# Kernel optimization log

Measured on AMD Instinct MI355X. Metric: run time of the kernel, lower is better.

Reference implementation:

```python
import jax, jax.numpy as jnp
import numpy as np

LN_EPS = 1e-5


def setup_inputs() -> dict:
    key = jax.random.key(0)
    ks = jax.random.split(key, 8)
    B, DIM = 65536, 768
    feat = jax.random.normal(ks[0], (B, 2, DIM), dtype=jnp.float32)
    s = 1.0 / np.sqrt(DIM)
    W_int = jax.random.uniform(ks[1], (9, DIM), minval=-s, maxval=s, dtype=jnp.float32)
    W_stim = jax.random.uniform(ks[2], (9, DIM), minval=-s, maxval=s, dtype=jnp.float32)
    trans = jax.random.uniform(ks[3], (9, 9, 9), dtype=jnp.float32)  # torch.rand init
    ln_w = jnp.ones((9,), dtype=jnp.float32)
    ln_b = jnp.zeros((9,), dtype=jnp.float32)
    so = 1.0 / np.sqrt(18)
    W_out = jax.random.uniform(ks[4], (9, 18), minval=-so, maxval=so, dtype=jnp.float32)
    b_out = jax.random.uniform(ks[5], (9,), minval=-so, maxval=so, dtype=jnp.float32)
    return {"feat": feat, "W_int": W_int, "W_stim": W_stim, "trans": trans,
            "ln_w": ln_w, "ln_b": ln_b, "W_out": W_out, "b_out": b_out}


def reference(feat, W_int, W_stim, trans, ln_w, ln_b, W_out, b_out):
    # last_feat = intensity(feat[:,0,:]); this_feat = stimulation(feat[:,1,:])
    last = feat[:, 0, :] @ W_int.T   # [B, 9]
    this = feat[:, 1, :] @ W_stim.T  # [B, 9]
    # per-sample: temp[a,k] = sum_j last[j]*trans[a,j,k]; out[k] = sum_a this[a]*temp[a,k]
    # batched trilinear contraction replaces the Python loop:
    bil = jnp.einsum('ba,bj,ajk->bk', this, last, trans)  # [B, 9]
    # LayerNorm(9)
    mu = jnp.mean(bil, axis=-1, keepdims=True)
    var = jnp.mean(jnp.square(bil - mu), axis=-1, keepdims=True)
    ln = (bil - mu) * jax.lax.rsqrt(var + LN_EPS) * ln_w + ln_b
    cat = jnp.concatenate([this, ln], axis=1)  # [B, 18]
    return cat @ W_out.T + b_out  # [B, 9]
```

## Files before the change

kernel.cpp:

```cpp
#include <hip/hip_runtime.h>

#define LN_EPS 1e-5f

constexpr int DIM   = 768;
constexpr int R     = 4;
constexpr int WAVES = 8;
constexpr int BLOCK = WAVES * 64;

__launch_bounds__(BLOCK, 1)
__global__ void fused_concat_linear(const float* __restrict__ feat,
                                    const float* __restrict__ W_int,
                                    const float* __restrict__ W_stim,
                                    const float* __restrict__ trans,
                                    const float* __restrict__ ln_w,
                                    const float* __restrict__ ln_b,
                                    const float* __restrict__ W_out,
                                    const float* __restrict__ b_out,
                                    float* __restrict__ out,
                                    int B)
{
    __shared__ float sW[2 * 9 * DIM];
    __shared__ float sTr[729];
    __shared__ float sWo[162];
    __shared__ float sBo[9];
    __shared__ float sLw[9];
    __shared__ float sLb[9];

    const int tid = threadIdx.x;
    {
        const float4* srcI = (const float4*)W_int;
        const float4* srcS = (const float4*)W_stim;
        float4* dst = (float4*)sW;
        constexpr int NW4 = (9 * DIM) / 4;
        for (int i = tid; i < NW4; i += BLOCK) {
            dst[i]       = srcI[i];
            dst[i + NW4] = srcS[i];
        }
        for (int i = tid; i < 729; i += BLOCK) sTr[i] = trans[i];
        if (tid < 162) sWo[tid] = W_out[tid];
        if (tid < 9) { sBo[tid] = b_out[tid]; sLw[tid] = ln_w[tid]; sLb[tid] = ln_b[tid]; }
    }
    __syncthreads();

    const int lane = tid & 63;
    const int wave = tid >> 6;
    const int r0 = (blockIdx.x * WAVES + wave) * R;

    int rows[R];
#pragma unroll
    for (int r = 0; r < R; ++r) rows[r] = min(r0 + r, B - 1);

    float acc_i[R][9];
    float acc_s[R][9];
#pragma unroll
    for (int r = 0; r < R; ++r)
#pragma unroll
        for (int a = 0; a < 9; ++a) { acc_i[r][a] = 0.f; acc_s[r][a] = 0.f; }

#pragma unroll
    for (int t = 0; t < 3; ++t) {
        const int base = t * 256 + lane * 4;
        float4 f0[R], f1[R];
#pragma unroll
        for (int r = 0; r < R; ++r) {
            const float* p = feat + (size_t)rows[r] * (2 * DIM);
            f0[r] = *(const float4*)(p + base);
            f1[r] = *(const float4*)(p + DIM + base);
        }
#pragma unroll
        for (int a = 0; a < 9; ++a) {
            const float4 wi = *(const float4*)(sW + a * DIM + base);
            const float4 ws = *(const float4*)(sW + 9 * DIM + a * DIM + base);
#pragma unroll
            for (int r = 0; r < R; ++r) {
                float ai = acc_i[r][a];
                ai = fmaf(f0[r].x, wi.x, ai);
                ai = fmaf(f0[r].y, wi.y, ai);
                ai = fmaf(f0[r].z, wi.z, ai);
                ai = fmaf(f0[r].w, wi.w, ai);
                acc_i[r][a] = ai;
                float as = acc_s[r][a];
                as = fmaf(f1[r].x, ws.x, as);
                as = fmaf(f1[r].y, ws.y, as);
                as = fmaf(f1[r].z, ws.z, as);
                as = fmaf(f1[r].w, ws.w, as);
                acc_s[r][a] = as;
            }
        }
    }

#pragma unroll
    for (int off = 32; off > 0; off >>= 1) {
#pragma unroll
        for (int r = 0; r < R; ++r)
#pragma unroll
            for (int a = 0; a < 9; ++a) {
                acc_i[r][a] += __shfl_xor(acc_i[r][a], off, 64);
                acc_s[r][a] += __shfl_xor(acc_s[r][a], off, 64);
            }
    }

    int rr = lane / 9;
    const int k = lane - rr * 9;
    const bool active = (rr < R);
    if (!active) rr = 0;

    float thisv[9], lastv[9];
#pragma unroll
    for (int a = 0; a < 9; ++a) {
        float tv = acc_s[0][a], lv = acc_i[0][a];
        tv = (rr == 1) ? acc_s[1][a] : tv;  lv = (rr == 1) ? acc_i[1][a] : lv;
        tv = (rr == 2) ? acc_s[2][a] : tv;  lv = (rr == 2) ? acc_i[2][a] : lv;
        tv = (rr == 3) ? acc_s[3][a] : tv;  lv = (rr == 3) ? acc_i[3][a] : lv;
        thisv[a] = tv; lastv[a] = lv;
    }

    float bil = 0.f;
#pragma unroll
    for (int a = 0; a < 9; ++a) {
        const float ta = thisv[a];
#pragma unroll
        for (int j = 0; j < 9; ++j) {
            bil = fmaf(ta * lastv[j], sTr[a * 81 + j * 9 + k], bil);
        }
    }

    const int rbase = rr * 9;
    float bilv[9];
#pragma unroll
    for (int j = 0; j < 9; ++j) bilv[j] = __shfl(bil, rbase + j, 64);

    float mu = 0.f;
#pragma unroll
    for (int j = 0; j < 9; ++j) mu += bilv[j];
    mu *= (1.f / 9.f);
    float var = 0.f;
#pragma unroll
    for (int j = 0; j < 9; ++j) { const float d = bilv[j] - mu; var = fmaf(d, d, var); }
    var *= (1.f / 9.f);
    const float rs = rsqrtf(var + LN_EPS);

    float o = sBo[k];
#pragma unroll
    for (int a = 0; a < 9; ++a) o = fmaf(thisv[a], sWo[k * 18 + a], o);
#pragma unroll
    for (int j = 0; j < 9; ++j) {
        const float lnj = fmaf((bilv[j] - mu) * rs, sLw[j], sLb[j]);
        o = fmaf(lnj, sWo[k * 18 + 9 + j], o);
    }

    const int row = r0 + rr;
    if (active && row < B) out[(size_t)row * 9 + k] = o;
}

extern "C" void kernel_launch(void* const* d_in, const int* in_sizes, int n_in,
                              void* d_out, int out_size, void* d_ws, size_t ws_size,
                              hipStream_t stream) {
    const float* feat   = (const float*)d_in[0];
    const float* W_int  = (const float*)d_in[1];
    const float* W_stim = (const float*)d_in[2];
    const float* trans  = (const float*)d_in[3];
    const float* ln_w   = (const float*)d_in[4];
    const float* ln_b   = (const float*)d_in[5];
    const float* W_out  = (const float*)d_in[6];
    const float* b_out  = (const float*)d_in[7];
    float* out = (float*)d_out;

    const int B = in_sizes[0] / (2 * DIM);
    const int rows_per_block = WAVES * R;
    const int grid = (B + rows_per_block - 1) / rows_per_block;

    fused_concat_linear<<<grid, BLOCK, 0, stream>>>(
        feat, W_int, W_stim, trans, ln_w, ln_b, W_out, b_out, out, B);
}
```

Before: 597.5 us.

## Map one row per lane and split DIM across waves with scalar weight loads

Work is remapped so each lane owns one batch row and each of four waves handles a quarter of the feature dimension. The wave-uniform weight addresses let the compiler use scalar loads straight from global memory, so the weights are no longer staged in LDS. This removes the 55 KB LDS preload per block and the long cross-lane shuffle reduction. Partial sums are now combined through a small LDS buffer, and wave 0 runs the bilinear, LayerNorm and output stages per row. The tradeoff is that per-lane feature loads now stride by a full row, which may hurt coalescing and L1 efficiency, and the epilogue runs on only one wave.

Measured after the change: 561.0 us. 6.1% less time.

```diff
diff --git a/kernel.cpp b/kernel.cpp
--- a/kernel.cpp
+++ b/kernel.cpp
@@ -2,12 +2,14 @@
 
 #define LN_EPS 1e-5f
 
-constexpr int DIM   = 768;
-constexpr int R     = 4;
-constexpr int WAVES = 8;
-constexpr int BLOCK = WAVES * 64;
+constexpr int DIM    = 768;
+constexpr int NSPLIT = 4;
+constexpr int BLOCK  = NSPLIT * 64;
+constexpr int SEG    = DIM / NSPLIT;
+constexpr int C      = 32;
+constexpr int NCHUNK = SEG / C;
 
-__launch_bounds__(BLOCK, 1)
+__launch_bounds__(BLOCK, 4)
 __global__ void fused_concat_linear(const float* __restrict__ feat,
                                     const float* __restrict__ W_int,
                                     const float* __restrict__ W_stim,
@@ -19,138 +21,114 @@
                                     float* __restrict__ out,
                                     int B)
 {
-    __shared__ float sW[2 * 9 * DIM];
-    __shared__ float sTr[729];
-    __shared__ float sWo[162];
-    __shared__ float sBo[9];
-    __shared__ float sLw[9];
-    __shared__ float sLb[9];
+    __shared__ float sP[NSPLIT][18][64];
 
-    const int tid = threadIdx.x;
-    {
-        const float4* srcI = (const float4*)W_int;
-        const float4* srcS = (const float4*)W_stim;
-        float4* dst = (float4*)sW;
-        constexpr int NW4 = (9 * DIM) / 4;
-        for (int i = tid; i < NW4; i += BLOCK) {
-            dst[i]       = srcI[i];
-            dst[i + NW4] = srcS[i];
-        }
-        for (int i = tid; i < 729; i += BLOCK) sTr[i] = trans[i];
-        if (tid < 162) sWo[tid] = W_out[tid];
-        if (tid < 9) { sBo[tid] = b_out[tid]; sLw[tid] = ln_w[tid]; sLb[tid] = ln_b[tid]; }
-    }
-    __syncthreads();
+    const int lane = threadIdx.x & 63;
+    const int wave = __builtin_amdgcn_readfirstlane(threadIdx.x >> 6);
 
-    const int lane = tid & 63;
-    const int wave = tid >> 6;
-    const int r0 = (blockIdx.x * WAVES + wave) * R;
+    const int row = blockIdx.x * 64 + lane;
+    const int rr  = min(row, B - 1);
+    const float* frow = feat + (size_t)rr * (2 * DIM);
 
-    int rows[R];
+    float accL[9], accT[9];
 #pragma unroll
-    for (int r = 0; r < R; ++r) rows[r] = min(r0 + r, B - 1);
-
-    float acc_i[R][9];
-    float acc_s[R][9];
-#pragma unroll
-    for (int r = 0; r < R; ++r)
-#pragma unroll
-        for (int a = 0; a < 9; ++a) { acc_i[r][a] = 0.f; acc_s[r][a] = 0.f; }
+    for (int a = 0; a < 9; ++a) { accL[a] = 0.f; accT[a] = 0.f; }
 
 #pragma unroll
-    for (int t = 0; t < 3; ++t) {
-        const int base = t * 256 + lane * 4;
-        float4 f0[R], f1[R];
+    for (int ch = 0; ch < NCHUNK; ++ch) {
+        const int c0 = wave * SEG + ch * C;
+
+        float4 f0[8], f1[8];
 #pragma unroll
-        for (int r = 0; r < R; ++r) {
-            const float* p = feat + (size_t)rows[r] * (2 * DIM);
-            f0[r] = *(const float4*)(p + base);
-            f1[r] = *(const float4*)(p + DIM + base);
-        }
+        for (int m = 0; m < 8; ++m) f0[m] = *(const float4*)(frow + c0 + 4 * m);
+#pragma unroll
+        for (int m = 0; m < 8; ++m) f1[m] = *(const float4*)(frow + DIM + c0 + 4 * m);
+
 #pragma unroll
         for (int a = 0; a < 9; ++a) {
-            const float4 wi = *(const float4*)(sW + a * DIM + base);
-            const float4 ws = *(const float4*)(sW + 9 * DIM + a * DIM + base);
+            const float* wi = W_int  + a * DIM + c0;
+            const float* ws = W_stim + a * DIM + c0;
+            float sL = accL[a];
 #pragma unroll
-            for (int r = 0; r < R; ++r) {
-                float ai = acc_i[r][a];
-                ai = fmaf(f0[r].x, wi.x, ai);
-                ai = fmaf(f0[r].y, wi.y, ai);
-                ai = fmaf(f0[r].z, wi.z, ai);
-                ai = fmaf(f0[r].w, wi.w, ai);
-                acc_i[r][a] = ai;
-                float as = acc_s[r][a];
-                as = fmaf(f1[r].x, ws.x, as);
-                as = fmaf(f1[r].y, ws.y, as);
-                as = fmaf(f1[r].z, ws.z, as);
-                as = fmaf(f1[r].w, ws.w, as);
-                acc_s[r][a] = as;
+            for (int m = 0; m < 8; ++m) {
+                const float4 w = *(const float4*)(wi + 4 * m);
+                sL = fmaf(f0[m].x, w.x, sL);
+                sL = fmaf(f0[m].y, w.y, sL);
+                sL = fmaf(f0[m].z, w.z, sL);
+                sL = fmaf(f0[m].w, w.w, sL);
             }
+            accL[a] = sL;
+            float sT = accT[a];
+#pragma unroll
+            for (int m = 0; m < 8; ++m) {
+                const float4 w = *(const float4*)(ws + 4 * m);
+                sT = fmaf(f1[m].x, w.x, sT);
+                sT = fmaf(f1[m].y, w.y, sT);
+                sT = fmaf(f1[m].z, w.z, sT);
+                sT = fmaf(f1[m].w, w.w, sT);
+            }
+            accT[a] = sT;
         }
     }
 
 #pragma unroll
-    for (int off = 32; off > 0; off >>= 1) {
+    for (int a = 0; a < 9; ++a) {
+        sP[wave][a][lane]     = accL[a];
+        sP[wave][9 + a][lane] = accT[a];
+    }
+    __syncthreads();
+
+    if (wave == 0) {
+        float lastv[9], thisv[9];
 #pragma unroll
-        for (int r = 0; r < R; ++r)
+        for (int a = 0; a < 9; ++a) {
+            lastv[a] = ((sP[0][a][lane]     + sP[1][a][lane])
+                      + (sP[2][a][lane]     + sP[3][a][lane]));
+            thisv[a] = ((sP[0][9 + a][lane] + sP[1][9 + a][lane])
+                      + (sP[2][9 + a][lane] + sP[3][9 + a][lane]));
+        }
+
+        float bil[9];
 #pragma unroll
-            for (int a = 0; a < 9; ++a) {
-                acc_i[r][a] += __shfl_xor(acc_i[r][a], off, 64);
-                acc_s[r][a] += __shfl_xor(acc_s[r][a], off, 64);
+        for (int k = 0; k < 9; ++k) bil[k] = 0.f;
+#pragma unroll
+        for (int a = 0; a < 9; ++a) {
+#pragma unroll
+            for (int j = 0; j < 9; ++j) {
+                const float p = thisv[a] * lastv[j];
+                const float* tp = trans + (a * 81 + j * 9);
+#pragma unroll
+                for (int k = 0; k < 9; ++k) bil[k] = fmaf(p, tp[k], bil[k]);
             }
-    }
+        }
 
-    int rr = lane / 9;
-    const int k = lane - rr * 9;
-    const bool active = (rr < R);
-    if (!active) rr = 0;
+        float mu = 0.f;
+#pragma unroll
+        for (int k = 0; k < 9; ++k) mu += bil[k];
+        mu *= (1.f / 9.f);
+        float var = 0.f;
+#pragma unroll
+        for (int k = 0; k < 9; ++k) { const float d = bil[k] - mu; var = fmaf(d, d, var); }
+        var *= (1.f / 9.f);
+        const float rs = rsqrtf(var + LN_EPS);
 
-    float thisv[9], lastv[9];
+        float lnv[9];
 #pragma unroll
-    for (int a = 0; a < 9; ++a) {
-        float tv = acc_s[0][a], lv = acc_i[0][a];
-        tv = (rr == 1) ? acc_s[1][a] : tv;  lv = (rr == 1) ? acc_i[1][a] : lv;
-        tv = (rr == 2) ? acc_s[2][a] : tv;  lv = (rr == 2) ? acc_i[2][a] : lv;
-        tv = (rr == 3) ? acc_s[3][a] : tv;  lv = (rr == 3) ? acc_i[3][a] : lv;
-        thisv[a] = tv; lastv[a] = lv;
-    }
+        for (int j = 0; j < 9; ++j)
+            lnv[j] = fmaf((bil[j] - mu) * rs, ln_w[j], ln_b[j]);
 
-    float bil = 0.f;
+        if (row < B) {
 #pragma unroll
-    for (int a = 0; a < 9; ++a) {
-        const float ta = thisv[a];
+            for (int i = 0; i < 9; ++i) {
+                float o = b_out[i];
 #pragma unroll
-        for (int j = 0; j < 9; ++j) {
-            bil = fmaf(ta * lastv[j], sTr[a * 81 + j * 9 + k], bil);
+                for (int a = 0; a < 9; ++a) o = fmaf(thisv[a], W_out[i * 18 + a], o);
+#pragma unroll
+                for (int j = 0; j < 9; ++j) o = fmaf(lnv[j], W_out[i * 18 + 9 + j], o);
+                out[(size_t)row * 9 + i] = o;
+            }
         }
     }
-
-    const int rbase = rr * 9;
-    float bilv[9];
-#pragma unroll
-    for (int j = 0; j < 9; ++j) bilv[j] = __shfl(bil, rbase + j, 64);
-
-    float mu = 0.f;
-#pragma unroll
-    for (int j = 0; j < 9; ++j) mu += bilv[j];
-    mu *= (1.f / 9.f);
-    float var = 0.f;
-#pragma unroll
-    for (int j = 0; j < 9; ++j) { const float d = bilv[j] - mu; var = fmaf(d, d, var); }
-    var *= (1.f / 9.f);
-    const float rs = rsqrtf(var + LN_EPS);
-
-    float o = sBo[k];
-#pragma unroll
-    for (int a = 0; a < 9; ++a) o = fmaf(thisv[a], sWo[k * 18 + a], o);
-#pragma unroll
-    for (int j = 0; j < 9; ++j) {
-        const float lnj = fmaf((bilv[j] - mu) * rs, sLw[j], sLb[j]);
-        o = fmaf(lnj, sWo[k * 18 + 9 + j], o);
-    }
-
-    const int row = r0 + rr;
-    if (active && row < B) out[(size_t)row * 9 + k] = o;
 }
 
 extern "C" void kernel_launch(void* const* d_in, const int* in_sizes, int n_in,
@@ -167,8 +145,7 @@
     float* out = (float*)d_out;
 
     const int B = in_sizes[0] / (2 * DIM);
-    const int rows_per_block = WAVES * R;
-    const int grid = (B + rows_per_block - 1) / rows_per_block;
+    const int grid = (B + 63) / 64;
 
     fused_concat_linear<<<grid, BLOCK, 0, stream>>>(
         feat, W_int, W_stim, trans, ln_w, ln_b, W_out, b_out, out, B);
```
